# Optimization experiments

Hardware: AMD Instinct MI355X
Metric: run time of the kernel (lower is better)

## Reference

```python
import jax, jax.numpy as jnp
import numpy as np

E, K, D = 50000, 8, 256
NH = 4
HD = D // NH
SCALE = HD ** -0.5
EPS = 1e-8


def setup_inputs() -> dict:
    key = jax.random.key(0)
    ks = jax.random.split(key, 16)
    p = lambda k, shp: (jax.random.normal(k, shp, dtype=jnp.float32) * 0.02)
    return {
        "x_i": jax.random.normal(ks[0], (E, D), dtype=jnp.float32),
        "x_j": jax.random.normal(ks[1], (E, D), dtype=jnp.float32),
        "h_seq_i": jax.random.normal(ks[2], (E, K, D), dtype=jnp.float32),
        "h_seq_j": jax.random.normal(ks[3], (E, K, D), dtype=jnp.float32),
        "edge_emb": jax.random.normal(ks[4], (E, D), dtype=jnp.float32),
        "Wq": p(ks[5], (D, D)), "bq": jnp.zeros((D,), jnp.float32),
        "Wk": p(ks[6], (D, D)), "bk": jnp.zeros((D,), jnp.float32),
        "We1": p(ks[7], (D, D // 2)), "be1": jnp.zeros((D // 2,), jnp.float32),
        "We2": p(ks[8], (D // 2, 1)), "be2": jnp.zeros((1,), jnp.float32),
        "Wo1": p(ks[9], (3, 16)), "bo1": jnp.zeros((16,), jnp.float32),
        "Wo2": p(ks[10], (16, 1)), "bo2": jnp.zeros((1,), jnp.float32),
    }


def reference(x_i, x_j, h_seq_i, h_seq_j, edge_emb,
              Wq, bq, Wk, bk, We1, be1, We2, be2, Wo1, bo1, Wo2, bo2):
    # (A) attribute alignment: cosine similarity mapped to (0,1)
    num = jnp.sum(x_i * x_j, axis=-1)
    den = jnp.maximum(jnp.linalg.norm(x_i, axis=-1), EPS) * \
          jnp.maximum(jnp.linalg.norm(x_j, axis=-1), EPS)
    attr_score = (num / den + 1.0) / 2.0  # [E]

    # (B) activity alignment: tiny cross-attention, mean of softmax diagonal
    Q = (jnp.einsum('ekd,df->ekf', h_seq_i, Wq) + bq).reshape(E, K, NH, HD)
    Kv = (jnp.einsum('ekd,df->ekf', h_seq_j, Wk) + bk).reshape(E, K, NH, HD)
    scores = jnp.einsum('eqhd,ekhd->ehqk', Q, Kv) * SCALE  # [E,NH,K,K]
    attn = jax.nn.softmax(scores, axis=-1)
    diag = jnp.diagonal(attn, axis1=-2, axis2=-1)  # [E,NH,K]
    activity_score = diag.mean(axis=(-1, -2))  # [E]

    # (C) edge plausibility MLP (exact GELU as in torch default)
    h = jax.nn.gelu(edge_emb @ We1 + be1, approximate=False)
    edge_score = jax.nn.sigmoid((h @ We2 + be2)[..., 0])  # [E]

    signals = jnp.stack([attr_score, activity_score, edge_score], axis=-1)  # [E,3]
    out = jax.nn.gelu(signals @ Wo1 + bo1, approximate=False) @ Wo2 + bo2
    return jax.nn.sigmoid(out[..., 0])  # [E]
```

## Files before the change

kernel.cpp:

```cpp
#include <hip/hip_runtime.h>

#define E_TOT   50000
#define DD      256
#define TE      4
#define NGROUP  (E_TOT / TE)
#define SCALE_V 0.125f

typedef __attribute__((ext_vector_type(4))) float f32x4;
typedef __attribute__((ext_vector_type(8))) short short8;

__device__ __forceinline__ unsigned short f2bf(float f) {
    unsigned u = __float_as_uint(f);
    u += 0x7fffu + ((u >> 16) & 1u);
    return (unsigned short)(u >> 16);
}
__device__ __forceinline__ float gelu_exact(float x) {
    return 0.5f * x * (1.0f + erff(x * 0.70710678118654752440f));
}
__device__ __forceinline__ float sigmoidf(float x) {
    return 1.0f / (1.0f + __expf(-x));
}

__global__ void prep_weights(const float* __restrict__ Wq,
                             const float* __restrict__ Wk,
                             const float* __restrict__ We1,
                             unsigned short* __restrict__ wqT,
                             unsigned short* __restrict__ wkT,
                             unsigned short* __restrict__ w1T) {
    int i = blockIdx.x * 256 + threadIdx.x;
    if (i < 65536) {
        int k = i >> 8, n = i & 255;
        wqT[n * 256 + k] = f2bf(Wq[i]);
    } else if (i < 131072) {
        int j = i - 65536;
        int k = j >> 8, n = j & 255;
        wkT[n * 256 + k] = f2bf(Wk[j]);
    } else {
        int j = i - 131072;
        int k = j >> 7, n = j & 127;
        w1T[n * 256 + k] = f2bf(We1[j]);
    }
}

__device__ __forceinline__ void proj_gemm(const unsigned short (*A)[260],
                                          const unsigned short* __restrict__ Wt,
                                          f32x4 acc[2][4], int lr, int lq, int w) {
    #pragma unroll
    for (int ks = 0; ks < 8; ++ks) {
        short8 a0 = *(const short8*)&A[lr][ks * 32 + lq * 8];
        short8 a1 = *(const short8*)&A[16 + lr][ks * 32 + lq * 8];
        #pragma unroll
        for (int n = 0; n < 4; ++n) {
            const int col = (w * 4 + n) * 16 + lr;
            short8 bv = *(const short8*)(Wt + col * 256 + ks * 32 + lq * 8);
            acc[0][n] = __builtin_amdgcn_mfma_f32_16x16x32_bf16(a0, bv, acc[0][n], 0, 0, 0);
            acc[1][n] = __builtin_amdgcn_mfma_f32_16x16x32_bf16(a1, bv, acc[1][n], 0, 0, 0);
        }
    }
}

__device__ __forceinline__ void writeback(unsigned short (*T)[260],
                                          const f32x4 acc[2][4],
                                          const float* __restrict__ bias,
                                          int lr, int lq, int w) {
    #pragma unroll
    for (int n = 0; n < 4; ++n) {
        const int col = (w * 4 + n) * 16 + lr;
        const float bs = bias[col];
        #pragma unroll
        for (int m = 0; m < 2; ++m) {
            #pragma unroll
            for (int v = 0; v < 4; ++v) {
                const int row = m * 16 + lq * 4 + v;
                T[row][col] = f2bf(acc[m][n][v] + bs);
            }
        }
    }
}

__global__ __launch_bounds__(256, 4)
void fused_all(const float* __restrict__ x_i,
               const float* __restrict__ x_j,
               const float* __restrict__ h_i,
               const float* __restrict__ h_j,
               const float* __restrict__ emb,
               const unsigned short* __restrict__ wqT,
               const unsigned short* __restrict__ wkT,
               const unsigned short* __restrict__ w1T,
               const float* __restrict__ bq,
               const float* __restrict__ bk,
               const float* __restrict__ be1,
               const float* __restrict__ We2,
               const float* __restrict__ be2,
               const float* __restrict__ Wo1,
               const float* __restrict__ bo1,
               const float* __restrict__ Wo2,
               const float* __restrict__ bo2,
               float* __restrict__ out) {
    __shared__ unsigned short bufHI[32][260];
    __shared__ unsigned short bufHJ[32][260];
    __shared__ float sEdgeP[4][4];

    const int t  = threadIdx.x;
    const int w  = t >> 6;
    const int l  = t & 63;
    const int lr = l & 15, lq = l >> 4;
    const int g  = blockIdx.x;
    const int e  = g * TE + w;
    const size_t hbase = (size_t)g * (TE * 8 * DD);

    f32x4 xa = *(const f32x4*)(x_i + (size_t)e * DD + l * 4);
    f32x4 xb = *(const f32x4*)(x_j + (size_t)e * DD + l * 4);
    f32x4 si[8], sj[8];
    #pragma unroll
    for (int i = 0; i < 8; ++i)
        si[i] = *(const f32x4*)(h_i + hbase + (size_t)(i * 256 + t) * 4);
    #pragma unroll
    for (int i = 0; i < 8; ++i)
        sj[i] = *(const f32x4*)(h_j + hbase + (size_t)(i * 256 + t) * 4);
    __builtin_amdgcn_sched_barrier(0);

    #pragma unroll
    for (int i = 0; i < 8; ++i) {
        const int f = i * 256 + t;
        *(ushort4*)&bufHI[f >> 6][(f & 63) * 4] =
            make_ushort4(f2bf(si[i][0]), f2bf(si[i][1]), f2bf(si[i][2]), f2bf(si[i][3]));
    }
    #pragma unroll
    for (int i = 0; i < 8; ++i) {
        const int f = i * 256 + t;
        *(ushort4*)&bufHJ[f >> 6][(f & 63) * 4] =
            make_ushort4(f2bf(sj[i][0]), f2bf(sj[i][1]), f2bf(sj[i][2]), f2bf(sj[i][3]));
    }
    float cd = xa[0]*xb[0] + xa[1]*xb[1] + xa[2]*xb[2] + xa[3]*xb[3];
    float ci = xa[0]*xa[0] + xa[1]*xa[1] + xa[2]*xa[2] + xa[3]*xa[3];
    float cj = xb[0]*xb[0] + xb[1]*xb[1] + xb[2]*xb[2] + xb[3]*xb[3];
    __syncthreads();

    {
        f32x4 accE[2] = {};
        const float* embrow = emb + ((size_t)g * TE + (lr & 3)) * DD;
        #pragma unroll
        for (int ks = 0; ks < 8; ++ks) {
            f32x4 e0 = *(const f32x4*)(embrow + ks * 32 + lq * 8);
            f32x4 e1 = *(const f32x4*)(embrow + ks * 32 + lq * 8 + 4);
            short8 ae;
            ae[0] = (short)f2bf(e0[0]); ae[1] = (short)f2bf(e0[1]);
            ae[2] = (short)f2bf(e0[2]); ae[3] = (short)f2bf(e0[3]);
            ae[4] = (short)f2bf(e1[0]); ae[5] = (short)f2bf(e1[1]);
            ae[6] = (short)f2bf(e1[2]); ae[7] = (short)f2bf(e1[3]);
            #pragma unroll
            for (int n = 0; n < 2; ++n) {
                const int col = w * 32 + n * 16 + lr;
                short8 bv = *(const short8*)(w1T + col * 256 + ks * 32 + lq * 8);
                accE[n] = __builtin_amdgcn_mfma_f32_16x16x32_bf16(ae, bv, accE[n], 0, 0, 0);
            }
        }
        float p[4] = {0.f, 0.f, 0.f, 0.f};
        #pragma unroll
        for (int n = 0; n < 2; ++n) {
            const int col = w * 32 + n * 16 + lr;
            const float b1 = be1[col], w2 = We2[col];
            #pragma unroll
            for (int v = 0; v < 4; ++v)
                p[v] += gelu_exact(accE[n][v] + b1) * w2;
        }
        #pragma unroll
        for (int off = 1; off < 16; off <<= 1) {
            #pragma unroll
            for (int v = 0; v < 4; ++v) p[v] += __shfl_xor(p[v], off);
        }
        if (l == 0) {
            sEdgeP[w][0] = p[0]; sEdgeP[w][1] = p[1];
            sEdgeP[w][2] = p[2]; sEdgeP[w][3] = p[3];
        }
    }

    f32x4 accQ[2][4] = {};
    f32x4 accK[2][4] = {};
    proj_gemm(bufHI, wqT, accQ, lr, lq, w);
    proj_gemm(bufHJ, wkT, accK, lr, lq, w);
    __syncthreads();
    writeback(bufHI, accQ, bq, lr, lq, w);
    writeback(bufHJ, accK, bk, lr, lq, w);
    __syncthreads();

    float contrib = 0.f;
    #pragma unroll
    for (int h = 0; h < 4; ++h) {
        f32x4 s = {};
        #pragma unroll
        for (int ks = 0; ks < 2; ++ks) {
            short8 a = *(const short8*)&bufHJ[w * 8 + (lr & 7)][h * 64 + ks * 32 + lq * 8];
            short8 b = *(const short8*)&bufHI[w * 8 + (lr & 7)][h * 64 + ks * 32 + lq * 8];
            s = __builtin_amdgcn_mfma_f32_16x16x32_bf16(a, b, s, 0, 0, 0);
        }
        float sc[4];
        #pragma unroll
        for (int v = 0; v < 4; ++v) sc[v] = s[v] * SCALE_V;
        float m4 = fmaxf(fmaxf(sc[0], sc[1]), fmaxf(sc[2], sc[3]));
        float mx = fmaxf(m4, __shfl_xor(m4, 16));
        float pe[4], ps = 0.f;
        #pragma unroll
        for (int v = 0; v < 4; ++v) { pe[v] = __expf(sc[v] - mx); ps += pe[v]; }
        float tot = ps + __shfl_xor(ps, 16);
        float pd = 0.f;
        #pragma unroll
        for (int v = 0; v < 4; ++v)
            pd = (((lq * 4 + v) & 7) == (lr & 7)) ? pe[v] : pd;
        if (lr < 8 && lq < 2) contrib += pd / tot;
    }

    #pragma unroll
    for (int off = 1; off < 64; off <<= 1) {
        contrib += __shfl_xor(contrib, off);
        cd += __shfl_xor(cd, off);
        ci += __shfl_xor(ci, off);
        cj += __shfl_xor(cj, off);
    }
    const float act  = contrib * (1.0f / 32.0f);
    const float attr = (cd / (fmaxf(sqrtf(ci), 1e-8f) * fmaxf(sqrtf(cj), 1e-8f))
                        + 1.0f) * 0.5f;
    const float es = sigmoidf(sEdgeP[0][w] + sEdgeP[1][w] + sEdgeP[2][w] +
                              sEdgeP[3][w] + be2[0]);

    float r = 0.f;
    if (l < 16) {
        float z = attr * Wo1[l] + act * Wo1[16 + l] + es * Wo1[32 + l] + bo1[l];
        r = gelu_exact(z) * Wo2[l];
    }
    r += __shfl_xor(r, 1);
    r += __shfl_xor(r, 2);
    r += __shfl_xor(r, 4);
    r += __shfl_xor(r, 8);
    if (l == 0) out[e] = sigmoidf(r + bo2[0]);
}

extern "C" void kernel_launch(void* const* d_in, const int* in_sizes, int n_in,
                              void* d_out, int out_size, void* d_ws, size_t ws_size,
                              hipStream_t stream) {
    const float* x_i  = (const float*)d_in[0];
    const float* x_j  = (const float*)d_in[1];
    const float* h_i  = (const float*)d_in[2];
    const float* h_j  = (const float*)d_in[3];
    const float* emb  = (const float*)d_in[4];
    const float* Wq   = (const float*)d_in[5];
    const float* bq   = (const float*)d_in[6];
    const float* Wk   = (const float*)d_in[7];
    const float* bk   = (const float*)d_in[8];
    const float* We1  = (const float*)d_in[9];
    const float* be1  = (const float*)d_in[10];
    const float* We2  = (const float*)d_in[11];
    const float* be2  = (const float*)d_in[12];
    const float* Wo1  = (const float*)d_in[13];
    const float* bo1  = (const float*)d_in[14];
    const float* Wo2  = (const float*)d_in[15];
    const float* bo2  = (const float*)d_in[16];
    float* out = (float*)d_out;

    unsigned short* wqT = (unsigned short*)d_ws;
    unsigned short* wkT = wqT + 65536;
    unsigned short* w1T = wkT + 65536;

    prep_weights<<<640, 256, 0, stream>>>(Wq, Wk, We1, wqT, wkT, w1T);
    fused_all<<<NGROUP, 256, 0, stream>>>(x_i, x_j, h_i, h_j, emb,
                                          wqT, wkT, w1T,
                                          bq, bk, be1, We2, be2,
                                          Wo1, bo1, Wo2, bo2, out);
}
```

Baseline: 655.7 us.

## Issue all global loads up front with staged vmcnt waits and stage emb in LDS

All global loads (h_i, h_j, x_i, x_j and the edge-embedding rows) are now issued together through inline-asm dwordx4 loads, with explicit vmcnt waits so the LDS conversion of h_i can begin while the later loads are still in flight. The embedding tile is staged once in shared memory instead of being re-read from global memory by each wave. The Q and K projections are split into separate scopes to cut peak register pressure, and the GELU/edge reduction moves after them. Launch bounds drop from 4 to 3 blocks per CU, which allows more registers per thread but lowers occupancy, and the larger LDS footprint further limits residency.

```diff
diff --git a/kernel.cpp b/kernel.cpp
--- a/kernel.cpp
+++ b/kernel.cpp
@@ -20,6 +20,14 @@
 __device__ __forceinline__ float sigmoidf(float x) {
     return 1.0f / (1.0f + __expf(-x));
 }
+
+__device__ __forceinline__ f32x4 aload(const float* p) {
+    f32x4 r;
+    asm volatile("global_load_dwordx4 %0, %1, off" : "=v"(r) : "v"(p));
+    return r;
+}
+#define WAITV(N) do { asm volatile("s_waitcnt vmcnt(" #N ")" ::: "memory"); \
+                      __builtin_amdgcn_sched_barrier(0); } while (0)
 
 __global__ void prep_weights(const float* __restrict__ Wq,
                              const float* __restrict__ Wk,
@@ -78,7 +86,7 @@
     }
 }
 
-__global__ __launch_bounds__(256, 4)
+__global__ __launch_bounds__(256, 3)
 void fused_all(const float* __restrict__ x_i,
                const float* __restrict__ x_j,
                const float* __restrict__ h_i,
@@ -97,8 +105,9 @@
                const float* __restrict__ Wo2,
                const float* __restrict__ bo2,
                float* __restrict__ out) {
-    __shared__ unsigned short bufHI[32][260];
-    __shared__ unsigned short bufHJ[32][260];
+    __shared__ unsigned short tI[32][260];
+    __shared__ unsigned short tJ[32][260];
+    __shared__ float sEmb[TE][DD];
     __shared__ float sEdgeP[4][4];
 
     const int t  = threadIdx.x;
@@ -109,41 +118,45 @@
     const int e  = g * TE + w;
     const size_t hbase = (size_t)g * (TE * 8 * DD);
 
-    f32x4 xa = *(const f32x4*)(x_i + (size_t)e * DD + l * 4);
-    f32x4 xb = *(const f32x4*)(x_j + (size_t)e * DD + l * 4);
     f32x4 si[8], sj[8];
     #pragma unroll
     for (int i = 0; i < 8; ++i)
-        si[i] = *(const f32x4*)(h_i + hbase + (size_t)(i * 256 + t) * 4);
+        si[i] = aload(h_i + hbase + (size_t)(i * 256 + t) * 4);
     #pragma unroll
     for (int i = 0; i < 8; ++i)
-        sj[i] = *(const f32x4*)(h_j + hbase + (size_t)(i * 256 + t) * 4);
+        sj[i] = aload(h_j + hbase + (size_t)(i * 256 + t) * 4);
+    f32x4 xa = aload(x_i + (size_t)e * DD + l * 4);
+    f32x4 xb = aload(x_j + (size_t)e * DD + l * 4);
+    f32x4 em = aload(emb + ((size_t)g * TE + (t >> 6)) * DD + (t & 63) * 4);
     __builtin_amdgcn_sched_barrier(0);
 
+    WAITV(11);
     #pragma unroll
     for (int i = 0; i < 8; ++i) {
         const int f = i * 256 + t;
-        *(ushort4*)&bufHI[f >> 6][(f & 63) * 4] =
+        *(ushort4*)&tI[f >> 6][(f & 63) * 4] =
             make_ushort4(f2bf(si[i][0]), f2bf(si[i][1]), f2bf(si[i][2]), f2bf(si[i][3]));
     }
+    WAITV(3);
     #pragma unroll
     for (int i = 0; i < 8; ++i) {
         const int f = i * 256 + t;
-        *(ushort4*)&bufHJ[f >> 6][(f & 63) * 4] =
+        *(ushort4*)&tJ[f >> 6][(f & 63) * 4] =
             make_ushort4(f2bf(sj[i][0]), f2bf(sj[i][1]), f2bf(sj[i][2]), f2bf(sj[i][3]));
     }
+    WAITV(0);
+    *(f32x4*)&sEmb[t >> 6][(t & 63) * 4] = em;
     float cd = xa[0]*xb[0] + xa[1]*xb[1] + xa[2]*xb[2] + xa[3]*xb[3];
     float ci = xa[0]*xa[0] + xa[1]*xa[1] + xa[2]*xa[2] + xa[3]*xa[3];
     float cj = xb[0]*xb[0] + xb[1]*xb[1] + xb[2]*xb[2] + xb[3]*xb[3];
     __syncthreads();
 
-    {
-        f32x4 accE[2] = {};
-        const float* embrow = emb + ((size_t)g * TE + (lr & 3)) * DD;
+    f32x4 accE[2] = {};
+    {
         #pragma unroll
         for (int ks = 0; ks < 8; ++ks) {
-            f32x4 e0 = *(const f32x4*)(embrow + ks * 32 + lq * 8);
-            f32x4 e1 = *(const f32x4*)(embrow + ks * 32 + lq * 8 + 4);
+            f32x4 e0 = *(const f32x4*)&sEmb[lr & 3][ks * 32 + lq * 8];
+            f32x4 e1 = *(const f32x4*)&sEmb[lr & 3][ks * 32 + lq * 8 + 4];
             short8 ae;
             ae[0] = (short)f2bf(e0[0]); ae[1] = (short)f2bf(e0[1]);
             ae[2] = (short)f2bf(e0[2]); ae[3] = (short)f2bf(e0[3]);
@@ -156,6 +169,20 @@
                 accE[n] = __builtin_amdgcn_mfma_f32_16x16x32_bf16(ae, bv, accE[n], 0, 0, 0);
             }
         }
+    }
+    {
+        f32x4 accQ[2][4] = {};
+        proj_gemm(tI, wqT, accQ, lr, lq, w);
+        __syncthreads();
+        writeback(tI, accQ, bq, lr, lq, w);
+    }
+    {
+        f32x4 accK[2][4] = {};
+        proj_gemm(tJ, wkT, accK, lr, lq, w);
+        __syncthreads();
+        writeback(tJ, accK, bk, lr, lq, w);
+    }
+    {
         float p[4] = {0.f, 0.f, 0.f, 0.f};
         #pragma unroll
         for (int n = 0; n < 2; ++n) {
@@ -175,14 +202,6 @@
             sEdgeP[w][2] = p[2]; sEdgeP[w][3] = p[3];
         }
     }
-
-    f32x4 accQ[2][4] = {};
-    f32x4 accK[2][4] = {};
-    proj_gemm(bufHI, wqT, accQ, lr, lq, w);
-    proj_gemm(bufHJ, wkT, accK, lr, lq, w);
-    __syncthreads();
-    writeback(bufHI, accQ, bq, lr, lq, w);
-    writeback(bufHJ, accK, bk, lr, lq, w);
     __syncthreads();
 
     float contrib = 0.f;
@@ -191,8 +210,8 @@
         f32x4 s = {};
         #pragma unroll
         for (int ks = 0; ks < 2; ++ks) {
-            short8 a = *(const short8*)&bufHJ[w * 8 + (lr & 7)][h * 64 + ks * 32 + lq * 8];
-            short8 b = *(const short8*)&bufHI[w * 8 + (lr & 7)][h * 64 + ks * 32 + lq * 8];
+            short8 a = *(const short8*)&tJ[w * 8 + (lr & 7)][h * 64 + ks * 32 + lq * 8];
+            short8 b = *(const short8*)&tI[w * 8 + (lr & 7)][h * 64 + ks * 32 + lq * 8];
             s = __builtin_amdgcn_mfma_f32_16x16x32_bf16(a, b, s, 0, 0, 0);
         }
         float sc[4];
```

Result: faster. 607.5 us (-7.4%).

## Pre-convert activations to bf16 MFMA fragments and DMA them into LDS

Applied to the files above, without the earlier changes.

Adds a separate pass that converts h_seq_i, h_seq_j and edge_emb to bf16, with h laid out in MFMA fragment order in workspace. The main kernel then loads these fragments straight into LDS using global_load_lds, and processes 8 edges per workgroup instead of 4 to reuse the weight fragments. The aim is to remove the in-kernel conversion and register staging. The cost is an extra full write and re-read of the activations through HBM, plus a very large workspace requirement.

```diff
diff --git a/kernel.cpp b/kernel.cpp
--- a/kernel.cpp
+++ b/kernel.cpp
@@ -2,9 +2,12 @@
 
 #define E_TOT   50000
 #define DD      256
-#define TE      4
-#define NGROUP  (E_TOT / TE)
+#define EPG     8
+#define NWG     (E_TOT / EPG)
 #define SCALE_V 0.125f
+
+#define NHCHUNK 12800000
+#define NECHUNK 1600000
 
 typedef __attribute__((ext_vector_type(4))) float f32x4;
 typedef __attribute__((ext_vector_type(8))) short short8;
@@ -19,6 +22,13 @@
 }
 __device__ __forceinline__ float sigmoidf(float x) {
     return 1.0f / (1.0f + __expf(-x));
+}
+
+__device__ __forceinline__ void dma16(const void* g, void* lds) {
+    const int lane = threadIdx.x & 63;
+    auto gp = (const __attribute__((address_space(1))) char*)g + lane * 16;
+    auto lp = (__attribute__((address_space(3))) char*)lds;
+    __builtin_amdgcn_global_load_lds(gp, lp, 16, 0, 0);
 }
 
 __global__ void prep_weights(const float* __restrict__ Wq,
@@ -42,33 +52,57 @@
     }
 }
 
-__device__ __forceinline__ void proj_gemm(const unsigned short (*A)[260],
-                                          const unsigned short* __restrict__ Wt,
-                                          f32x4 acc[2][4], int lr, int lq, int w) {
-    #pragma unroll
-    for (int ks = 0; ks < 8; ++ks) {
-        short8 a0 = *(const short8*)&A[lr][ks * 32 + lq * 8];
-        short8 a1 = *(const short8*)&A[16 + lr][ks * 32 + lq * 8];
-        #pragma unroll
-        for (int n = 0; n < 4; ++n) {
-            const int col = (w * 4 + n) * 16 + lr;
-            short8 bv = *(const short8*)(Wt + col * 256 + ks * 32 + lq * 8);
-            acc[0][n] = __builtin_amdgcn_mfma_f32_16x16x32_bf16(a0, bv, acc[0][n], 0, 0, 0);
-            acc[1][n] = __builtin_amdgcn_mfma_f32_16x16x32_bf16(a1, bv, acc[1][n], 0, 0, 0);
-        }
-    }
-}
-
-__device__ __forceinline__ void writeback(unsigned short (*T)[260],
-                                          const f32x4 acc[2][4],
-                                          const float* __restrict__ bias,
-                                          int lr, int lq, int w) {
+__global__ void conv_frag(const float* __restrict__ hi,
+                          const float* __restrict__ hj,
+                          const float* __restrict__ emb,
+                          unsigned short* __restrict__ fi,
+                          unsigned short* __restrict__ fj,
+                          unsigned short* __restrict__ ebf) {
+    const int nthr = gridDim.x * blockDim.x;
+    const int tid  = blockIdx.x * blockDim.x + threadIdx.x;
+
+    for (int c = tid; c < NHCHUNK; c += nthr) {
+        const int g  = c >> 10;
+        const int r  = c & 1023;
+        const int ks = r >> 7, m = (r >> 6) & 1, l = r & 63;
+        const size_t row = (size_t)g * 32 + m * 16 + (l & 15);
+        const int    col = ks * 32 + (l >> 4) * 8;
+        const float* pi = hi + row * DD + col;
+        const float* pj = hj + row * DD + col;
+        f32x4 a0 = *(const f32x4*)pi;
+        f32x4 a1 = *(const f32x4*)(pi + 4);
+        f32x4 b0 = *(const f32x4*)pj;
+        f32x4 b1 = *(const f32x4*)(pj + 4);
+        *(ushort4*)(fi + (size_t)c * 8)     =
+            make_ushort4(f2bf(a0[0]), f2bf(a0[1]), f2bf(a0[2]), f2bf(a0[3]));
+        *(ushort4*)(fi + (size_t)c * 8 + 4) =
+            make_ushort4(f2bf(a1[0]), f2bf(a1[1]), f2bf(a1[2]), f2bf(a1[3]));
+        *(ushort4*)(fj + (size_t)c * 8)     =
+            make_ushort4(f2bf(b0[0]), f2bf(b0[1]), f2bf(b0[2]), f2bf(b0[3]));
+        *(ushort4*)(fj + (size_t)c * 8 + 4) =
+            make_ushort4(f2bf(b1[0]), f2bf(b1[1]), f2bf(b1[2]), f2bf(b1[3]));
+    }
+    for (int c = tid; c < NECHUNK; c += nthr) {
+        const float* p = emb + (size_t)c * 8;
+        f32x4 a0 = *(const f32x4*)p;
+        f32x4 a1 = *(const f32x4*)(p + 4);
+        *(ushort4*)(ebf + (size_t)c * 8)     =
+            make_ushort4(f2bf(a0[0]), f2bf(a0[1]), f2bf(a0[2]), f2bf(a0[3]));
+        *(ushort4*)(ebf + (size_t)c * 8 + 4) =
+            make_ushort4(f2bf(a1[0]), f2bf(a1[1]), f2bf(a1[2]), f2bf(a1[3]));
+    }
+}
+
+__device__ __forceinline__ void writeback4(unsigned short (*T)[260],
+                                           const f32x4 acc[4][4],
+                                           const float* __restrict__ bias,
+                                           int lr, int lq, int w) {
     #pragma unroll
     for (int n = 0; n < 4; ++n) {
         const int col = (w * 4 + n) * 16 + lr;
         const float bs = bias[col];
         #pragma unroll
-        for (int m = 0; m < 2; ++m) {
+        for (int m = 0; m < 4; ++m) {
             #pragma unroll
             for (int v = 0; v < 4; ++v) {
                 const int row = m * 16 + lq * 4 + v;
@@ -78,77 +112,72 @@
     }
 }
 
-__global__ __launch_bounds__(256, 4)
-void fused_all(const float* __restrict__ x_i,
-               const float* __restrict__ x_j,
-               const float* __restrict__ h_i,
-               const float* __restrict__ h_j,
-               const float* __restrict__ emb,
-               const unsigned short* __restrict__ wqT,
-               const unsigned short* __restrict__ wkT,
-               const unsigned short* __restrict__ w1T,
-               const float* __restrict__ bq,
-               const float* __restrict__ bk,
-               const float* __restrict__ be1,
-               const float* __restrict__ We2,
-               const float* __restrict__ be2,
-               const float* __restrict__ Wo1,
-               const float* __restrict__ bo1,
-               const float* __restrict__ Wo2,
-               const float* __restrict__ bo2,
-               float* __restrict__ out) {
-    __shared__ unsigned short bufHI[32][260];
-    __shared__ unsigned short bufHJ[32][260];
-    __shared__ float sEdgeP[4][4];
+__global__ __launch_bounds__(256, 2)
+void fused_tile(const float* __restrict__ x_i,
+                const float* __restrict__ x_j,
+                const unsigned short* __restrict__ fi,
+                const unsigned short* __restrict__ fj,
+                const unsigned short* __restrict__ ebf,
+                const unsigned short* __restrict__ wqT,
+                const unsigned short* __restrict__ wkT,
+                const unsigned short* __restrict__ w1T,
+                const float* __restrict__ bq,
+                const float* __restrict__ bk,
+                const float* __restrict__ be1,
+                const float* __restrict__ We2,
+                const float* __restrict__ be2,
+                const float* __restrict__ Wo1,
+                const float* __restrict__ bo1,
+                const float* __restrict__ Wo2,
+                const float* __restrict__ bo2,
+                float* __restrict__ out) {
+    __shared__ __align__(16) unsigned char lds[66560 + 128];
+    unsigned short (*tQ)[260] = (unsigned short (*)[260])lds;
+    unsigned short (*tK)[260] = (unsigned short (*)[260])(lds + 33280);
+    unsigned char* fiS = lds;
+    unsigned char* fjS = lds + 33280;
+    float* sEdgeP = (float*)(lds + 66560);
 
     const int t  = threadIdx.x;
     const int w  = t >> 6;
     const int l  = t & 63;
     const int lr = l & 15, lq = l >> 4;
-    const int g  = blockIdx.x;
-    const int e  = g * TE + w;
-    const size_t hbase = (size_t)g * (TE * 8 * DD);
-
-    f32x4 xa = *(const f32x4*)(x_i + (size_t)e * DD + l * 4);
-    f32x4 xb = *(const f32x4*)(x_j + (size_t)e * DD + l * 4);
-    f32x4 si[8], sj[8];
+    const int b  = blockIdx.x;
+
     #pragma unroll
     for (int i = 0; i < 8; ++i)
-        si[i] = *(const f32x4*)(h_i + hbase + (size_t)(i * 256 + t) * 4);
+        dma16((const char*)fi + (size_t)b * 32768 + w * 8192 + i * 1024,
+              fiS + w * 8192 + i * 1024);
     #pragma unroll
     for (int i = 0; i < 8; ++i)
-        sj[i] = *(const f32x4*)(h_j + hbase + (size_t)(i * 256 + t) * 4);
-    __builtin_amdgcn_sched_barrier(0);
-
-    #pragma unroll
-    for (int i = 0; i < 8; ++i) {
-        const int f = i * 256 + t;
-        *(ushort4*)&bufHI[f >> 6][(f & 63) * 4] =
-            make_ushort4(f2bf(si[i][0]), f2bf(si[i][1]), f2bf(si[i][2]), f2bf(si[i][3]));
-    }
-    #pragma unroll
-    for (int i = 0; i < 8; ++i) {
-        const int f = i * 256 + t;
-        *(ushort4*)&bufHJ[f >> 6][(f & 63) * 4] =
-            make_ushort4(f2bf(sj[i][0]), f2bf(sj[i][1]), f2bf(sj[i][2]), f2bf(sj[i][3]));
-    }
-    float cd = xa[0]*xb[0] + xa[1]*xb[1] + xa[2]*xb[2] + xa[3]*xb[3];
-    float ci = xa[0]*xa[0] + xa[1]*xa[1] + xa[2]*xa[2] + xa[3]*xa[3];
-    float cj = xb[0]*xb[0] + xb[1]*xb[1] + xb[2]*xb[2] + xb[3]*xb[3];
-    __syncthreads();
+        dma16((const char*)fj + (size_t)b * 32768 + w * 8192 + i * 1024,
+              fjS + w * 8192 + i * 1024);
+
+    float attr[2];
+    #pragma unroll
+    for (int ee = 0; ee < 2; ++ee) {
+        const int e = b * EPG + 2 * w + ee;
+        f32x4 xa = *(const f32x4*)(x_i + (size_t)e * DD + l * 4);
+        f32x4 xb = *(const f32x4*)(x_j + (size_t)e * DD + l * 4);
+        float cd = xa[0]*xb[0] + xa[1]*xb[1] + xa[2]*xb[2] + xa[3]*xb[3];
+        float ci = xa[0]*xa[0] + xa[1]*xa[1] + xa[2]*xa[2] + xa[3]*xa[3];
+        float cj = xb[0]*xb[0] + xb[1]*xb[1] + xb[2]*xb[2] + xb[3]*xb[3];
+        #pragma unroll
+        for (int off = 1; off < 64; off <<= 1) {
+            cd += __shfl_xor(cd, off);
+            ci += __shfl_xor(ci, off);
+            cj += __shfl_xor(cj, off);
+        }
+        attr[ee] = (cd / (fmaxf(sqrtf(ci), 1e-8f) * fmaxf(sqrtf(cj), 1e-8f))
+                    + 1.0f) * 0.5f;
+    }
 
     {
         f32x4 accE[2] = {};
-        const float* embrow = emb + ((size_t)g * TE + (lr & 3)) * DD;
+        const unsigned short* er = ebf + ((size_t)b * EPG + (lr & 7)) * 256;
         #pragma unroll
         for (int ks = 0; ks < 8; ++ks) {
-            f32x4 e0 = *(const f32x4*)(embrow + ks * 32 + lq * 8);
-            f32x4 e1 = *(const f32x4*)(embrow + ks * 32 + lq * 8 + 4);
-            short8 ae;
-            ae[0] = (short)f2bf(e0[0]); ae[1] = (short)f2bf(e0[1]);
-            ae[2] = (short)f2bf(e0[2]); ae[3] = (short)f2bf(e0[3]);
-            ae[4] = (short)f2bf(e1[0]); ae[5] = (short)f2bf(e1[1]);
-            ae[6] = (short)f2bf(e1[2]); ae[7] = (short)f2bf(e1[3]);
+            short8 ae = *(const short8*)(er + ks * 32 + lq * 8);
             #pragma unroll
             for (int n = 0; n < 2; ++n) {
                 const int col = w * 32 + n * 16 + lr;
@@ -171,69 +200,107 @@
             for (int v = 0; v < 4; ++v) p[v] += __shfl_xor(p[v], off);
         }
         if (l == 0) {
-            sEdgeP[w][0] = p[0]; sEdgeP[w][1] = p[1];
-            sEdgeP[w][2] = p[2]; sEdgeP[w][3] = p[3];
-        }
-    }
-
-    f32x4 accQ[2][4] = {};
-    f32x4 accK[2][4] = {};
-    proj_gemm(bufHI, wqT, accQ, lr, lq, w);
-    proj_gemm(bufHJ, wkT, accK, lr, lq, w);
+            sEdgeP[w * 8 + 0] = p[0]; sEdgeP[w * 8 + 1] = p[1];
+            sEdgeP[w * 8 + 2] = p[2]; sEdgeP[w * 8 + 3] = p[3];
+        }
+        if (l == 16) {
+            sEdgeP[w * 8 + 4] = p[0]; sEdgeP[w * 8 + 5] = p[1];
+            sEdgeP[w * 8 + 6] = p[2]; sEdgeP[w * 8 + 7] = p[3];
+        }
+    }
     __syncthreads();
-    writeback(bufHI, accQ, bq, lr, lq, w);
-    writeback(bufHJ, accK, bk, lr, lq, w);
+
+    f32x4 accQ[4][4] = {};
+    #pragma unroll
+    for (int ks = 0; ks < 8; ++ks) {
+        short8 bv[4];
+        #pragma unroll
+        for (int n = 0; n < 4; ++n)
+            bv[n] = *(const short8*)(wqT + ((w * 4 + n) * 16 + lr) * 256 + ks * 32 + lq * 8);
+        #pragma unroll
+        for (int m = 0; m < 4; ++m) {
+            short8 av = *(const short8*)(fiS + (m >> 1) * 16384 + ks * 2048 +
+                                         (m & 1) * 1024 + l * 16);
+            #pragma unroll
+            for (int n = 0; n < 4; ++n)
+                accQ[m][n] = __builtin_amdgcn_mfma_f32_16x16x32_bf16(av, bv[n], accQ[m][n], 0, 0, 0);
+        }
+    }
     __syncthreads();
-
-    float contrib = 0.f;
-    #pragma unroll
-    for (int h = 0; h < 4; ++h) {
-        f32x4 s = {};
-        #pragma unroll
-        for (int ks = 0; ks < 2; ++ks) {
-            short8 a = *(const short8*)&bufHJ[w * 8 + (lr & 7)][h * 64 + ks * 32 + lq * 8];
-            short8 b = *(const short8*)&bufHI[w * 8 + (lr & 7)][h * 64 + ks * 32 + lq * 8];
-            s = __builtin_amdgcn_mfma_f32_16x16x32_bf16(a, b, s, 0, 0, 0);
-        }
-        float sc[4];
-        #pragma unroll
-        for (int v = 0; v < 4; ++v) sc[v] = s[v] * SCALE_V;
-        float m4 = fmaxf(fmaxf(sc[0], sc[1]), fmaxf(sc[2], sc[3]));
-        float mx = fmaxf(m4, __shfl_xor(m4, 16));
-        float pe[4], ps = 0.f;
-        #pragma unroll
-        for (int v = 0; v < 4; ++v) { pe[v] = __expf(sc[v] - mx); ps += pe[v]; }
-        float tot = ps + __shfl_xor(ps, 16);
-        float pd = 0.f;
-        #pragma unroll
-        for (int v = 0; v < 4; ++v)
-            pd = (((lq * 4 + v) & 7) == (lr & 7)) ? pe[v] : pd;
-        if (lr < 8 && lq < 2) contrib += pd / tot;
-    }
-
+    writeback4(tQ, accQ, bq, lr, lq, w);
+
+    f32x4 accK[4][4] = {};
+    #pragma unroll
+    for (int ks = 0; ks < 8; ++ks) {
+        short8 bv[4];
+        #pragma unroll
+        for (int n = 0; n < 4; ++n)
+            bv[n] = *(const short8*)(wkT + ((w * 4 + n) * 16 + lr) * 256 + ks * 32 + lq * 8);
+        #pragma unroll
+        for (int m = 0; m < 4; ++m) {
+            short8 av = *(const short8*)(fjS + (m >> 1) * 16384 + ks * 2048 +
+                                         (m & 1) * 1024 + l * 16);
+            #pragma unroll
+            for (int n = 0; n < 4; ++n)
+                accK[m][n] = __builtin_amdgcn_mfma_f32_16x16x32_bf16(av, bv[n], accK[m][n], 0, 0, 0);
+        }
+    }
+    __syncthreads();
+    writeback4(tK, accK, bk, lr, lq, w);
+    __syncthreads();
+
+    float contrib[2] = {0.f, 0.f};
+    #pragma unroll
+    for (int ee = 0; ee < 2; ++ee) {
+        const int rowb = (2 * w + ee) * 8 + (lr & 7);
+        #pragma unroll
+        for (int h = 0; h < 4; ++h) {
+            f32x4 s = {};
+            #pragma unroll
+            for (int ks = 0; ks < 2; ++ks) {
+                short8 a = *(const short8*)&tK[rowb][h * 64 + ks * 32 + lq * 8];
+                short8 bb = *(const short8*)&tQ[rowb][h * 64 + ks * 32 + lq * 8];
+                s = __builtin_amdgcn_mfma_f32_16x16x32_bf16(a, bb, s, 0, 0, 0);
+            }
+            float sc[4];
+            #pragma unroll
+            for (int v = 0; v < 4; ++v) sc[v] = s[v] * SCALE_V;
+            float m4 = fmaxf(fmaxf(sc[0], sc[1]), fmaxf(sc[2], sc[3]));
+            float mx = fmaxf(m4, __shfl_xor(m4, 16));
+            float pe[4], ps = 0.f;
+            #pragma unroll
+            for (int v = 0; v < 4; ++v) { pe[v] = __expf(sc[v] - mx); ps += pe[v]; }
+            float tot = ps + __shfl_xor(ps, 16);
+            float pd = 0.f;
+            #pragma unroll
+            for (int v = 0; v < 4; ++v)
+                pd = (((lq * 4 + v) & 7) == (lr & 7)) ? pe[v] : pd;
+            if (lr < 8 && lq < 2) contrib[ee] += pd / tot;
+        }
+    }
     #pragma unroll
     for (int off = 1; off < 64; off <<= 1) {
-        contrib += __shfl_xor(contrib, off);
-        cd += __shfl_xor(cd, off);
-        ci += __shfl_xor(ci, off);
-        cj += __shfl_xor(cj, off);
-    }
-    const float act  = contrib * (1.0f / 32.0f);
-    const float attr = (cd / (fmaxf(sqrtf(ci), 1e-8f) * fmaxf(sqrtf(cj), 1e-8f))
-                        + 1.0f) * 0.5f;
-    const float es = sigmoidf(sEdgeP[0][w] + sEdgeP[1][w] + sEdgeP[2][w] +
-                              sEdgeP[3][w] + be2[0]);
-
-    float r = 0.f;
-    if (l < 16) {
-        float z = attr * Wo1[l] + act * Wo1[16 + l] + es * Wo1[32 + l] + bo1[l];
-        r = gelu_exact(z) * Wo2[l];
-    }
-    r += __shfl_xor(r, 1);
-    r += __shfl_xor(r, 2);
-    r += __shfl_xor(r, 4);
-    r += __shfl_xor(r, 8);
-    if (l == 0) out[e] = sigmoidf(r + bo2[0]);
+        contrib[0] += __shfl_xor(contrib[0], off);
+        contrib[1] += __shfl_xor(contrib[1], off);
+    }
+
+    #pragma unroll
+    for (int ee = 0; ee < 2; ++ee) {
+        const int eloc = 2 * w + ee;
+        const float act = contrib[ee] * (1.0f / 32.0f);
+        const float es  = sigmoidf(sEdgeP[0 * 8 + eloc] + sEdgeP[1 * 8 + eloc] +
+                                   sEdgeP[2 * 8 + eloc] + sEdgeP[3 * 8 + eloc] + be2[0]);
+        float r = 0.f;
+        if (l < 16) {
+            float z = attr[ee] * Wo1[l] + act * Wo1[16 + l] + es * Wo1[32 + l] + bo1[l];
+            r = gelu_exact(z) * Wo2[l];
+        }
+        r += __shfl_xor(r, 1);
+        r += __shfl_xor(r, 2);
+        r += __shfl_xor(r, 4);
+        r += __shfl_xor(r, 8);
+        if (l == 0) out[b * EPG + eloc] = sigmoidf(r + bo2[0]);
+    }
 }
 
 extern "C" void kernel_launch(void* const* d_in, const int* in_sizes, int n_in,
@@ -261,10 +328,14 @@
     unsigned short* wqT = (unsigned short*)d_ws;
     unsigned short* wkT = wqT + 65536;
     unsigned short* w1T = wkT + 65536;
+    unsigned short* ebf = w1T + 32768;
+    unsigned short* fi  = ebf + 12800000;
+    unsigned short* fj  = fi + 102400000;
 
     prep_weights<<<640, 256, 0, stream>>>(Wq, Wk, We1, wqT, wkT, w1T);
-    fused_all<<<NGROUP, 256, 0, stream>>>(x_i, x_j, h_i, h_j, emb,
-                                          wqT, wkT, w1T,
-                                          bq, bk, be1, We2, be2,
-                                          Wo1, bo1, Wo2, bo2, out);
-}
+    conv_frag<<<2048, 256, 0, stream>>>(h_i, h_j, emb, fi, fj, ebf);
+    fused_tile<<<NWG, 256, 0, stream>>>(x_i, x_j, fi, fj, ebf,
+                                        wqT, wkT, w1T,
+                                        bq, bk, be1, We2, be2,
+                                        Wo1, bo1, Wo2, bo2, out);
+}
```

Result: slower. 674.8 us (+2.9%).
